# Optimization experiments

Hardware: AMD Instinct MI355X
Metric: run time of the kernel (lower is better)

## Reference

```python
import jax, jax.numpy as jnp
import numpy as np

B, I, H, T = 256, 256, 512, 400


def setup_inputs() -> dict:
    key = jax.random.key(0)
    k1, k2, k3, k4, k5 = jax.random.split(key, 5)
    s = 1.0 / np.sqrt(H)  # PyTorch LSTMCell init scale (values only matter for realism)
    return {
        "x": jax.random.normal(k1, (B, I, T), dtype=jnp.float32),
        "w_ih": jax.random.normal(k2, (4 * H, I), dtype=jnp.float32) * s,
        "w_hh": jax.random.normal(k3, (4 * H, H), dtype=jnp.float32) * s,
        "b_ih": jax.random.normal(k4, (4 * H,), dtype=jnp.float32) * s,
        "b_hh": jax.random.normal(k5, (4 * H,), dtype=jnp.float32) * s,
    }


def reference(x, w_ih, w_hh, b_ih, b_hh):
    # x: [B, I, T] -> time-major [T, B, I]
    x_t = jnp.transpose(x, (2, 0, 1))
    # Precompute input-side gate contributions (batched GEMM, parallel over T)
    xg = jnp.einsum("tbi,gi->tbg", x_t, w_ih) + b_ih + b_hh  # [T, B, 4H]

    h0 = jnp.zeros((x.shape[0], w_hh.shape[1]), dtype=x.dtype)
    c0 = jnp.zeros_like(h0)

    def step(carry, xg_t):
        h, c = carry
        gates = xg_t + h @ w_hh.T  # [B, 4H]
        i, f, g, o = jnp.split(gates, 4, axis=-1)  # PyTorch gate order i,f,g,o
        i = jax.nn.sigmoid(i)
        f = jax.nn.sigmoid(f)
        g = jnp.tanh(g)
        o = jax.nn.sigmoid(o)
        c_new = f * c + i * g
        h_new = o * jnp.tanh(c_new)
        return (h_new, c_new), c_new

    (h_T, c_T), c_stack = jax.lax.scan(step, (h0, c0), xg)
    return c_stack  # [T, B, H] -- the per-step cell states the module stores
```

## Files before the change

### kernel.cpp

```cpp
#include <hip/hip_runtime.h>
#include <stdint.h>

#define TT 400
#define BB 256
#define II 256
#define HH 512
#define NG 2048

typedef __attribute__((ext_vector_type(8))) _Float16 half8;
typedef __attribute__((ext_vector_type(4))) float f32x4;
typedef __attribute__((ext_vector_type(4))) unsigned int u32x4;
typedef unsigned int u32;
typedef unsigned short u16;

static __device__ __forceinline__ u32 f2hbits(float f){
  union { _Float16 h; u16 u; } c; c.h = (_Float16)f; return (u32)c.u;
}

#define GLOAD16(gsrc, ldst) \
  __builtin_amdgcn_global_load_lds((const __attribute__((address_space(1))) void*)(gsrc), \
                                   (__attribute__((address_space(3))) void*)(ldst), 16, 0, 0)

__global__ __launch_bounds__(256) void k_prep_x(const float* __restrict__ x,
                                                u16* __restrict__ xT){
  __shared__ float tile[32][17];
  const int bid = blockIdx.x;
  const int tb = bid % 25, ib = (bid / 25) & 7, b = bid / 200;
  const int t0 = tb * 16, i0 = ib * 32;
  const int tl = threadIdx.x & 15, il = threadIdx.x >> 4;
  tile[il][tl]      = x[(size_t)(b * II + i0 + il) * TT + t0 + tl];
  tile[il + 16][tl] = x[(size_t)(b * II + i0 + il + 16) * TT + t0 + tl];
  __syncthreads();
  const int t_l = threadIdx.x >> 4, ip = threadIdx.x & 15;
  const u32 pack = f2hbits(tile[2 * ip][t_l]) | (f2hbits(tile[2 * ip + 1][t_l]) << 16);
  *(u32*)(xT + ((size_t)(t0 + t_l) * BB + b) * II + i0 + 2 * ip) = pack;
}

__global__ __launch_bounds__(256) void k_prep_w(const float* __restrict__ w_ih,
                                                u16* __restrict__ Wp){
  const size_t idx = (size_t)blockIdx.x * 256 + threadIdx.x;
  const float4 v = *(const float4*)(w_ih + idx * 4);
  uint2 o;
  o.x = f2hbits(v.x) | (f2hbits(v.y) << 16);
  o.y = f2hbits(v.z) | (f2hbits(v.w) << 16);
  *(uint2*)(Wp + idx * 4) = o;
}

__global__ __launch_bounds__(256) void k_gemm_xg(const u16* __restrict__ A,
                                                 const u16* __restrict__ B,
                                                 _Float16* __restrict__ xg){
  __shared__ char lds[65536];
  const int tid = threadIdx.x, w = tid >> 6, lane = tid & 63;
  const int nb = blockIdx.x & 15, mb = blockIdx.x >> 4;
  const size_t m0 = (size_t)mb * 128;
  const int n0 = nb * 128;
  const int lr = lane & 15, lh = lane >> 4;

  auto stage = [&](int it, int buf){
    const size_t kb = (size_t)it * 128;
    #pragma unroll
    for (int i2 = 0; i2 < 4; ++i2){
      const int u = w * 256 + i2 * 64 + lane;
      const int r = u >> 3, s = u & 7;
      const char* g = (const char*)A + (m0 + r) * 512 + kb + ((s ^ (r & 7)) << 4);
      char* l = lds + buf * 16384 + ((w * 256 + i2 * 64) << 4);
      GLOAD16(g, l);
    }
    #pragma unroll
    for (int i2 = 0; i2 < 4; ++i2){
      const int u = w * 256 + i2 * 64 + lane;
      const int r = u >> 3, s = u & 7;
      const char* g = (const char*)B + (size_t)(n0 + r) * 512 + kb + ((s ^ (r & 7)) << 4);
      char* l = lds + 32768 + buf * 16384 + ((w * 256 + i2 * 64) << 4);
      GLOAD16(g, l);
    }
  };

  f32x4 acc[4][4];
  #pragma unroll
  for (int i = 0; i < 4; ++i)
    #pragma unroll
    for (int j = 0; j < 4; ++j){ f32x4 z = {0.f,0.f,0.f,0.f}; acc[i][j] = z; }

  const int wm = (w & 1) * 64, wn = (w >> 1) * 64;
  stage(0, 0);
  for (int it = 0; it < 4; ++it){
    const int buf = it & 1;
    if (it < 3) stage(it + 1, buf ^ 1);
    __syncthreads();
    const char* lA = lds + buf * 16384;
    const char* lB = lds + 32768 + buf * 16384;
    #pragma unroll
    for (int ks = 0; ks < 2; ++ks){
      half8 a[4], b[4];
      const int s = ks * 4 + lh;
      #pragma unroll
      for (int mt = 0; mt < 4; ++mt){
        const int r = wm + mt * 16 + lr;
        a[mt] = *(const half8*)(lA + r * 128 + ((s ^ (r & 7)) << 4));
      }
      #pragma unroll
      for (int nt = 0; nt < 4; ++nt){
        const int r = wn + nt * 16 + lr;
        b[nt] = *(const half8*)(lB + r * 128 + ((s ^ (r & 7)) << 4));
      }
      #pragma unroll
      for (int mt = 0; mt < 4; ++mt)
        #pragma unroll
        for (int nt = 0; nt < 4; ++nt)
          acc[mt][nt] = __builtin_amdgcn_mfma_f32_16x16x32_f16(a[mt], b[nt], acc[mt][nt], 0, 0, 0);
    }
    __syncthreads();
  }
  #pragma unroll
  for (int mt = 0; mt < 4; ++mt)
    #pragma unroll
    for (int nt = 0; nt < 4; ++nt)
      #pragma unroll
      for (int r = 0; r < 4; ++r){
        const size_t row = m0 + wm + mt * 16 + lh * 4 + r;
        const int col = n0 + wn + nt * 16 + lr;
        xg[row * NG + col] = (_Float16)acc[mt][nt][r];
      }
}

__global__ __launch_bounds__(512) void k_lstm(const _Float16* __restrict__ xg,
    const float* __restrict__ w_hh, const float* __restrict__ b_ih,
    const float* __restrict__ b_hh, u16* __restrict__ hbuf_g,
    u32* __restrict__ cnt, float* __restrict__ out){
  extern __shared__ char lds[];
  char* Wl  = lds;
  char* hbA = lds + 131072;
  char* hbB = lds + 139264;
  float* gbA = (float*)(lds + 147456);
  float* gbB = (float*)(lds + 151552);

  const int tid = threadIdx.x, w = tid >> 6, lane = tid & 63;
  const int lr = lane & 15, lh = lane >> 4;
  const int gb = blockIdx.x >> 4, gn = blockIdx.x & 15;
  const int b0 = gb * 16, j0 = gn * 32;
  u32* flagA = cnt + gb * 128;
  u32* flagB = flagA + 64;

  for (int rep = 0; rep < 16; ++rep){
    const int u = rep * 512 + tid;
    const int row = u >> 6, u0 = u & 63;
    const int grow = ((row >> 5) << 9) + j0 + (row & 31);
    const float* src = w_hh + (size_t)grow * HH + u0 * 8;
    const float4 va = *(const float4*)src;
    const float4 vb = *(const float4*)(src + 4);
    union { _Float16 h[8]; u32x4 v; } p;
    p.h[0] = (_Float16)va.x; p.h[1] = (_Float16)va.y;
    p.h[2] = (_Float16)va.z; p.h[3] = (_Float16)va.w;
    p.h[4] = (_Float16)vb.x; p.h[5] = (_Float16)vb.y;
    p.h[6] = (_Float16)vb.z; p.h[7] = (_Float16)vb.w;
    *(u32x4*)(Wl + row * 1024 + ((u0 ^ (row & 7)) << 4)) = p.v;
  }
  const int sub  = tid >> 8;
  const int brow = (tid & 255) >> 5;
  const int jj   = tid & 31;
  float bias_[4];
  #pragma unroll
  for (int q = 0; q < 4; ++q) bias_[q] = b_ih[q * HH + j0 + jj] + b_hh[q * HH + j0 + jj];
  float c = 0.f;
  const int sr = tid >> 6, su = tid & 63;
  const int slds = sr * 1024 + ((su ^ (sr & 7)) << 4);
  __syncthreads();

  for (int t = 0; t < TT; ++t){
    const _Float16* xt = xg + (size_t)t * (BB * NG) + (size_t)(b0 + sub * 8 + brow) * NG + j0 + jj;
    u32 xv0, xv1, xv2, xv3;
    asm volatile(
      "global_load_ushort %0, %4, off\n\t"
      "global_load_ushort %1, %5, off\n\t"
      "global_load_ushort %2, %6, off\n\t"
      "global_load_ushort %3, %7, off"
      : "=&v"(xv0), "=&v"(xv1), "=&v"(xv2), "=&v"(xv3)
      : "v"(xt), "v"(xt + HH), "v"(xt + 2 * HH), "v"(xt + 3 * HH)
      : "memory");

    #pragma unroll
    for (int ss = 0; ss < 2; ++ss){
      u32* flag = ss ? flagB : flagA;
      char* hb = ss ? hbB : hbA;
      float* gbuf = ss ? gbB : gbA;
      if (t > 0){
        if (tid == 0){
          const u32 target = (u32)(16 * t);
          u32 v; int guard = 0;
          do {
            asm volatile("global_load_dword %0, %1, off sc0 sc1\n\t"
                         "s_waitcnt vmcnt(0)"
                         : "=v"(v) : "v"(flag) : "memory");
          } while (v < target && ++guard < (1 << 22));
        }
        __syncthreads();
        const char* gh = (const char*)hbuf_g + (size_t)((t - 1) & 1) * 262144
                       + (size_t)(b0 + ss * 8) * 1024 + sr * 1024 + su * 16;
        u32x4 hv;
        asm volatile("global_load_dwordx4 %0, %1, off sc0 sc1\n\t"
                     "s_waitcnt vmcnt(0)"
                     : "=v"(hv) : "v"(gh) : "memory");
        *(u32x4*)(hb + slds) = hv;
        __syncthreads();
        f32x4 ac0 = {0.f,0.f,0.f,0.f}, ac1 = {0.f,0.f,0.f,0.f};
        const int nr = w * 16 + lr;
        const int nbase = nr * 1024, nx = nr & 7, ax = lr & 7;
        const char* abase = hb + lr * 1024;
        #pragma unroll
        for (int m = 0; m < 16; m += 2){
          const int s0 = m * 4 + lh, s1 = s0 + 4;
          const half8 a0 = *(const half8*)(abase + ((s0 ^ ax) << 4));
          const half8 bv0 = *(const half8*)(Wl + nbase + ((s0 ^ nx) << 4));
          ac0 = __builtin_amdgcn_mfma_f32_16x16x32_f16(a0, bv0, ac0, 0, 0, 0);
          const half8 a1 = *(const half8*)(abase + ((s1 ^ ax) << 4));
          const half8 bv1 = *(const half8*)(Wl + nbase + ((s1 ^ nx) << 4));
          ac1 = __builtin_amdgcn_mfma_f32_16x16x32_f16(a1, bv1, ac1, 0, 0, 0);
        }
        const f32x4 acs = ac0 + ac1;
        if (lh < 2){
          #pragma unroll
          for (int r = 0; r < 4; ++r)
            gbuf[(w * 8 + lh * 4 + r) * 16 + lr] = acs[r];
        }
        __syncthreads();
      }
      float cnew = c, hn = 0.f;
      if (sub == ss){
        asm volatile("s_waitcnt vmcnt(0)" ::: "memory");
        asm volatile("" : "+v"(xv0), "+v"(xv1), "+v"(xv2), "+v"(xv3));
        float g4[4];
        union { u32 u; _Float16 h[2]; } cv;
        cv.u = xv0; g4[0] = (float)cv.h[0] + bias_[0];
        cv.u = xv1; g4[1] = (float)cv.h[0] + bias_[1];
        cv.u = xv2; g4[2] = (float)cv.h[0] + bias_[2];
        cv.u = xv3; g4[3] = (float)cv.h[0] + bias_[3];
        if (t > 0){
          #pragma unroll
          for (int q = 0; q < 4; ++q)
            g4[q] += gbuf[((q * 2 + (jj >> 4)) * 8 + brow) * 16 + (jj & 15)];
        }
        const float i_ = 1.f / (1.f + __expf(-g4[0]));
        const float f_ = 1.f / (1.f + __expf(-g4[1]));
        const float ea = __expf(-2.f * fabsf(g4[2]));
        const float g_ = __builtin_copysignf((1.f - ea) / (1.f + ea), g4[2]);
        const float o_ = 1.f / (1.f + __expf(-g4[3]));
        cnew = f_ * c + i_ * g_;
        c = cnew;
        const float eb = __expf(-2.f * fabsf(cnew));
        const float th = __builtin_copysignf((1.f - eb) / (1.f + eb), cnew);
        hn = o_ * th;
        if (t < TT - 1){
          u16* ph = hbuf_g + (size_t)(t & 1) * (BB * HH)
                  + (size_t)(b0 + ss * 8 + brow) * HH + j0 + jj;
          const u32 hv16 = f2hbits(hn);
          asm volatile("global_store_short %0, %1, off sc0 sc1"
                       :: "v"(ph), "v"(hv16) : "memory");
        }
      }
      if (t < TT - 1){
        asm volatile("s_waitcnt vmcnt(0)" ::: "memory");
        __syncthreads();
        if (tid == 0)
          asm volatile("global_atomic_add %0, %1, off sc1" :: "v"(flag), "v"(1u) : "memory");
      }
      if (sub == ss)
        out[(size_t)t * (BB * HH) + (size_t)(b0 + ss * 8 + brow) * HH + j0 + jj] = c;
    }
  }
}

extern "C" void kernel_launch(void* const* d_in, const int* in_sizes, int n_in,
                              void* d_out, int out_size, void* d_ws, size_t ws_size,
                              hipStream_t stream){
  const float* x    = (const float*)d_in[0];
  const float* w_ih = (const float*)d_in[1];
  const float* w_hh = (const float*)d_in[2];
  const float* b_ih = (const float*)d_in[3];
  const float* b_hh = (const float*)d_in[4];
  float* out = (float*)d_out;
  char* ws = (char*)d_ws;

  const size_t o_xg  = 0;
  const size_t o_xt  = 419430400;
  const size_t o_wp  = 471859200;
  const size_t o_h   = 472907776;
  const size_t o_cnt = 473432064;
  const size_t need  = 473440256;
  if (ws_size < need) return;

  _Float16* xg = (_Float16*)(ws + o_xg);
  u16* xt  = (u16*)(ws + o_xt);
  u16* wp  = (u16*)(ws + o_wp);
  u16* hb  = (u16*)(ws + o_h);
  u32* cnt = (u32*)(ws + o_cnt);

  hipMemsetAsync(cnt, 0, 8192, stream);
  hipLaunchKernelGGL(k_prep_x, dim3(51200), dim3(256), 0, stream, x, xt);
  hipLaunchKernelGGL(k_prep_w, dim3(512), dim3(256), 0, stream, w_ih, wp);
  hipLaunchKernelGGL(k_gemm_xg, dim3(12800), dim3(256), 0, stream, xt, wp, xg);
  hipLaunchKernelGGL(k_lstm, dim3(256), dim3(512), 155648, stream,
                     xg, w_hh, b_ih, b_hh, hb, cnt, out);
}
```

Baseline: 2.238 ms.

## Replace per-step counter barrier with timestep-tagged hidden-state polling

Each fp16 hidden value is now stored as a 32-bit word with the timestep packed into its upper half. Consumers poll their own slices until every tag matches, instead of one thread spinning on an atomic counter, then an extra block barrier and a separate load. The two 8-row half-steps per timestep merge into one 16-row step, and the counter memset and atomics go away. This removes inter-block signalling latency and barriers from the serial recurrence, at the cost of doubling the hidden-state exchange traffic. Correctness relies on stale tags in the workspace never matching the expected timestep.

```diff
diff --git a/kernel.cpp b/kernel.cpp
--- a/kernel.cpp
+++ b/kernel.cpp
@@ -126,21 +126,17 @@
 
 __global__ __launch_bounds__(512) void k_lstm(const _Float16* __restrict__ xg,
     const float* __restrict__ w_hh, const float* __restrict__ b_ih,
-    const float* __restrict__ b_hh, u16* __restrict__ hbuf_g,
-    u32* __restrict__ cnt, float* __restrict__ out){
+    const float* __restrict__ b_hh, u32* __restrict__ htag,
+    float* __restrict__ out){
   extern __shared__ char lds[];
-  char* Wl  = lds;
-  char* hbA = lds + 131072;
-  char* hbB = lds + 139264;
-  float* gbA = (float*)(lds + 147456);
-  float* gbB = (float*)(lds + 151552);
+  char* Wl = lds;
+  char* hb = lds + 131072;
+  float* gbuf = (float*)(lds + 147456);
 
   const int tid = threadIdx.x, w = tid >> 6, lane = tid & 63;
   const int lr = lane & 15, lh = lane >> 4;
   const int gb = blockIdx.x >> 4, gn = blockIdx.x & 15;
   const int b0 = gb * 16, j0 = gn * 32;
-  u32* flagA = cnt + gb * 128;
-  u32* flagB = flagA + 64;
 
   for (int rep = 0; rep < 16; ++rep){
     const int u = rep * 512 + tid;
@@ -156,19 +152,26 @@
     p.h[6] = (_Float16)vb.z; p.h[7] = (_Float16)vb.w;
     *(u32x4*)(Wl + row * 1024 + ((u0 ^ (row & 7)) << 4)) = p.v;
   }
-  const int sub  = tid >> 8;
-  const int brow = (tid & 255) >> 5;
+  const int brow = tid >> 5;
   const int jj   = tid & 31;
   float bias_[4];
   #pragma unroll
   for (int q = 0; q < 4; ++q) bias_[q] = b_ih[q * HH + j0 + jj] + b_hh[q * HH + j0 + jj];
   float c = 0.f;
-  const int sr = tid >> 6, su = tid & 63;
-  const int slds = sr * 1024 + ((su ^ (sr & 7)) << 4);
+  const int q = w >> 1, jb = w & 1;
+
+  const int u1 = tid, u2 = tid + 512;
+  const int r1 = u1 >> 6, c1 = u1 & 63;
+  const int r2 = u2 >> 6, c2 = u2 & 63;
+  const size_t gof1 = (size_t)(b0 + r1) * 512 + c1 * 8;
+  const size_t gof2 = (size_t)(b0 + r2) * 512 + c2 * 8;
+  const int lof1 = r1 * 1024 + ((c1 ^ (r1 & 7)) << 4);
+  const int lof2 = r2 * 1024 + ((c2 ^ (r2 & 7)) << 4);
+  u32* pst0 = htag + (size_t)(b0 + brow) * 512 + (j0 + jj);
   __syncthreads();
 
   for (int t = 0; t < TT; ++t){
-    const _Float16* xt = xg + (size_t)t * (BB * NG) + (size_t)(b0 + sub * 8 + brow) * NG + j0 + jj;
+    const _Float16* xt = xg + (size_t)t * (BB * NG) + (size_t)(b0 + brow) * NG + j0 + jj;
     u32 xv0, xv1, xv2, xv3;
     asm volatile(
       "global_load_ushort %0, %4, off\n\t"
@@ -179,94 +182,98 @@
       : "v"(xt), "v"(xt + HH), "v"(xt + 2 * HH), "v"(xt + 3 * HH)
       : "memory");
 
-    #pragma unroll
-    for (int ss = 0; ss < 2; ++ss){
-      u32* flag = ss ? flagB : flagA;
-      char* hb = ss ? hbB : hbA;
-      float* gbuf = ss ? gbB : gbA;
-      if (t > 0){
-        if (tid == 0){
-          const u32 target = (u32)(16 * t);
-          u32 v; int guard = 0;
-          do {
-            asm volatile("global_load_dword %0, %1, off sc0 sc1\n\t"
-                         "s_waitcnt vmcnt(0)"
-                         : "=v"(v) : "v"(flag) : "memory");
-          } while (v < target && ++guard < (1 << 22));
+    if (t > 0){
+      const u32* gbase = htag + (size_t)((t - 1) & 1) * 131072;
+      const u32* g1 = gbase + gof1;
+      const u32* g2 = gbase + gof2;
+      const u32 te = ((u32)t) << 16;
+      u32x4 a0, a1, d0, d1;
+      int need = 3, guard = 0;
+      do {
+        if (need & 1)
+          asm volatile("global_load_dwordx4 %0, %2, off sc0 sc1\n\t"
+                       "global_load_dwordx4 %1, %3, off sc0 sc1"
+                       : "=&v"(a0), "=&v"(a1) : "v"(g1), "v"(g1 + 4) : "memory");
+        if (need & 2)
+          asm volatile("global_load_dwordx4 %0, %2, off sc0 sc1\n\t"
+                       "global_load_dwordx4 %1, %3, off sc0 sc1"
+                       : "=&v"(d0), "=&v"(d1) : "v"(g2), "v"(g2 + 4) : "memory");
+        asm volatile("s_waitcnt vmcnt(0)" ::: "memory");
+        if (need & 1){
+          u32 m = (a0[0]^te)|(a0[1]^te)|(a0[2]^te)|(a0[3]^te)
+                 |(a1[0]^te)|(a1[1]^te)|(a1[2]^te)|(a1[3]^te);
+          if (!(m >> 16)) need &= ~1;
         }
-        __syncthreads();
-        const char* gh = (const char*)hbuf_g + (size_t)((t - 1) & 1) * 262144
-                       + (size_t)(b0 + ss * 8) * 1024 + sr * 1024 + su * 16;
-        u32x4 hv;
-        asm volatile("global_load_dwordx4 %0, %1, off sc0 sc1\n\t"
-                     "s_waitcnt vmcnt(0)"
-                     : "=v"(hv) : "v"(gh) : "memory");
-        *(u32x4*)(hb + slds) = hv;
-        __syncthreads();
-        f32x4 ac0 = {0.f,0.f,0.f,0.f}, ac1 = {0.f,0.f,0.f,0.f};
-        const int nr = w * 16 + lr;
-        const int nbase = nr * 1024, nx = nr & 7, ax = lr & 7;
-        const char* abase = hb + lr * 1024;
-        #pragma unroll
-        for (int m = 0; m < 16; m += 2){
-          const int s0 = m * 4 + lh, s1 = s0 + 4;
-          const half8 a0 = *(const half8*)(abase + ((s0 ^ ax) << 4));
-          const half8 bv0 = *(const half8*)(Wl + nbase + ((s0 ^ nx) << 4));
-          ac0 = __builtin_amdgcn_mfma_f32_16x16x32_f16(a0, bv0, ac0, 0, 0, 0);
-          const half8 a1 = *(const half8*)(abase + ((s1 ^ ax) << 4));
-          const half8 bv1 = *(const half8*)(Wl + nbase + ((s1 ^ nx) << 4));
-          ac1 = __builtin_amdgcn_mfma_f32_16x16x32_f16(a1, bv1, ac1, 0, 0, 0);
+        if (need & 2){
+          u32 m = (d0[0]^te)|(d0[1]^te)|(d0[2]^te)|(d0[3]^te)
+                 |(d1[0]^te)|(d1[1]^te)|(d1[2]^te)|(d1[3]^te);
+          if (!(m >> 16)) need &= ~2;
         }
-        const f32x4 acs = ac0 + ac1;
-        if (lh < 2){
-          #pragma unroll
-          for (int r = 0; r < 4; ++r)
-            gbuf[(w * 8 + lh * 4 + r) * 16 + lr] = acs[r];
-        }
-        __syncthreads();
+      } while (need && ++guard < (1 << 18));
+      u32x4 p1, p2;
+      p1[0] = (a0[0] & 0xffffu) | (a0[1] << 16);
+      p1[1] = (a0[2] & 0xffffu) | (a0[3] << 16);
+      p1[2] = (a1[0] & 0xffffu) | (a1[1] << 16);
+      p1[3] = (a1[2] & 0xffffu) | (a1[3] << 16);
+      p2[0] = (d0[0] & 0xffffu) | (d0[1] << 16);
+      p2[1] = (d0[2] & 0xffffu) | (d0[3] << 16);
+      p2[2] = (d1[0] & 0xffffu) | (d1[1] << 16);
+      p2[3] = (d1[2] & 0xffffu) | (d1[3] << 16);
+      *(u32x4*)(hb + lof1) = p1;
+      *(u32x4*)(hb + lof2) = p2;
+      __syncthreads();
+      f32x4 ac0 = {0.f,0.f,0.f,0.f}, ac1 = {0.f,0.f,0.f,0.f};
+      const int nrow = q * 32 + jb * 16 + lr;
+      const int nbase = nrow * 1024, nx = nrow & 7, ax = lr & 7;
+      const char* abase = hb + lr * 1024;
+      #pragma unroll
+      for (int ks = 0; ks < 16; ks += 2){
+        const int s0 = ks * 4 + lh, s1 = s0 + 4;
+        const half8 av0 = *(const half8*)(abase + ((s0 ^ ax) << 4));
+        const half8 bv0 = *(const half8*)(Wl + nbase + ((s0 ^ nx) << 4));
+        ac0 = __builtin_amdgcn_mfma_f32_16x16x32_f16(av0, bv0, ac0, 0, 0, 0);
+        const half8 av1 = *(const half8*)(abase + ((s1 ^ ax) << 4));
+        const half8 bv1 = *(const half8*)(Wl + nbase + ((s1 ^ nx) << 4));
+        ac1 = __builtin_amdgcn_mfma_f32_16x16x32_f16(av1, bv1, ac1, 0, 0, 0);
       }
-      float cnew = c, hn = 0.f;
-      if (sub == ss){
-        asm volatile("s_waitcnt vmcnt(0)" ::: "memory");
-        asm volatile("" : "+v"(xv0), "+v"(xv1), "+v"(xv2), "+v"(xv3));
-        float g4[4];
-        union { u32 u; _Float16 h[2]; } cv;
-        cv.u = xv0; g4[0] = (float)cv.h[0] + bias_[0];
-        cv.u = xv1; g4[1] = (float)cv.h[0] + bias_[1];
-        cv.u = xv2; g4[2] = (float)cv.h[0] + bias_[2];
-        cv.u = xv3; g4[3] = (float)cv.h[0] + bias_[3];
-        if (t > 0){
-          #pragma unroll
-          for (int q = 0; q < 4; ++q)
-            g4[q] += gbuf[((q * 2 + (jj >> 4)) * 8 + brow) * 16 + (jj & 15)];
-        }
-        const float i_ = 1.f / (1.f + __expf(-g4[0]));
-        const float f_ = 1.f / (1.f + __expf(-g4[1]));
-        const float ea = __expf(-2.f * fabsf(g4[2]));
-        const float g_ = __builtin_copysignf((1.f - ea) / (1.f + ea), g4[2]);
-        const float o_ = 1.f / (1.f + __expf(-g4[3]));
-        cnew = f_ * c + i_ * g_;
-        c = cnew;
-        const float eb = __expf(-2.f * fabsf(cnew));
-        const float th = __builtin_copysignf((1.f - eb) / (1.f + eb), cnew);
-        hn = o_ * th;
-        if (t < TT - 1){
-          u16* ph = hbuf_g + (size_t)(t & 1) * (BB * HH)
-                  + (size_t)(b0 + ss * 8 + brow) * HH + j0 + jj;
-          const u32 hv16 = f2hbits(hn);
-          asm volatile("global_store_short %0, %1, off sc0 sc1"
-                       :: "v"(ph), "v"(hv16) : "memory");
-        }
-      }
-      if (t < TT - 1){
-        asm volatile("s_waitcnt vmcnt(0)" ::: "memory");
-        __syncthreads();
-        if (tid == 0)
-          asm volatile("global_atomic_add %0, %1, off sc1" :: "v"(flag), "v"(1u) : "memory");
-      }
-      if (sub == ss)
-        out[(size_t)t * (BB * HH) + (size_t)(b0 + ss * 8 + brow) * HH + j0 + jj] = c;
-    }
+      const f32x4 acs = ac0 + ac1;
+      #pragma unroll
+      for (int r = 0; r < 4; ++r)
+        gbuf[(q * 16 + lh * 4 + r) * 32 + jb * 16 + lr] = acs[r];
+      __syncthreads();
+    }
+    asm volatile("s_waitcnt vmcnt(0)" ::: "memory");
+    asm volatile("" : "+v"(xv0), "+v"(xv1), "+v"(xv2), "+v"(xv3));
+
+    float g4[4];
+    {
+      union { u32 u; _Float16 h[2]; } cv;
+      cv.u = xv0; g4[0] = (float)cv.h[0] + bias_[0];
+      cv.u = xv1; g4[1] = (float)cv.h[0] + bias_[1];
+      cv.u = xv2; g4[2] = (float)cv.h[0] + bias_[2];
+      cv.u = xv3; g4[3] = (float)cv.h[0] + bias_[3];
+    }
+    if (t > 0){
+      #pragma unroll
+      for (int qq = 0; qq < 4; ++qq) g4[qq] += gbuf[(qq * 16 + brow) * 32 + jj];
+    }
+    const float i_ = 1.f / (1.f + __expf(-g4[0]));
+    const float f_ = 1.f / (1.f + __expf(-g4[1]));
+    const float ea = __expf(-2.f * fabsf(g4[2]));
+    const float g_ = __builtin_copysignf((1.f - ea) / (1.f + ea), g4[2]);
+    const float o_ = 1.f / (1.f + __expf(-g4[3]));
+    c = f_ * c + i_ * g_;
+    const float eb = __expf(-2.f * fabsf(c));
+    const float th = __builtin_copysignf((1.f - eb) / (1.f + eb), c);
+    const float hn = o_ * th;
+
+    if (t < TT - 1){
+      u32* ph = pst0 + (size_t)(t & 1) * 131072;
+      const u32 hv = f2hbits(hn) | ((u32)(t + 1) << 16);
+      asm volatile("global_store_dword %0, %1, off sc0 sc1"
+                   :: "v"(ph), "v"(hv) : "memory");
+    }
+    out[(size_t)t * (BB * HH) + (size_t)(b0 + brow) * HH + j0 + jj] = c;
   }
 }
 
@@ -285,20 +292,17 @@
   const size_t o_xt  = 419430400;
   const size_t o_wp  = 471859200;
   const size_t o_h   = 472907776;
-  const size_t o_cnt = 473432064;
-  const size_t need  = 473440256;
+  const size_t need  = 473956352;
   if (ws_size < need) return;
 
   _Float16* xg = (_Float16*)(ws + o_xg);
   u16* xt  = (u16*)(ws + o_xt);
   u16* wp  = (u16*)(ws + o_wp);
-  u16* hb  = (u16*)(ws + o_h);
-  u32* cnt = (u32*)(ws + o_cnt);
-
-  hipMemsetAsync(cnt, 0, 8192, stream);
+  u32* ht  = (u32*)(ws + o_h);
+
   hipLaunchKernelGGL(k_prep_x, dim3(51200), dim3(256), 0, stream, x, xt);
   hipLaunchKernelGGL(k_prep_w, dim3(512), dim3(256), 0, stream, w_ih, wp);
   hipLaunchKernelGGL(k_gemm_xg, dim3(12800), dim3(256), 0, stream, xt, wp, xg);
   hipLaunchKernelGGL(k_lstm, dim3(256), dim3(512), 155648, stream,
-                     xg, w_hh, b_ih, b_hh, hb, cnt, out);
-}
+                     xg, w_hh, b_ih, b_hh, ht, out);
+}
```

After: 1.817 ms. -18.8%, faster.
